# Kernel optimization log

Hardware: AMD Instinct MI355X
Metric: run time of the kernel (lower is better)

The kernel has to match this reference:

```python
import jax, jax.numpy as jnp
import numpy as np

EPS = 1e-6

def setup_inputs() -> dict:
    key = jax.random.key(0)
    k1, k2 = jax.random.split(key)
    S, B, H, F = 2048, 4, 2048, 8192
    x = jax.random.normal(k1, (S, B, H), dtype=jnp.float32)
    scale = jnp.ones((H,), dtype=jnp.float32)
    ln_bias = jnp.zeros((H,), dtype=jnp.float32)
    kernel = jax.random.normal(k2, (H, F), dtype=jnp.float32) * 0.02  # ~variance_scaling fan_in
    return {"x": x, "scale": scale, "ln_bias": ln_bias, "kernel": kernel}

def reference(x, scale, ln_bias, kernel):
    # LayerNorm over last (hidden) axis, stats in fp32
    mu = jnp.mean(x, axis=-1, keepdims=True)
    var = jnp.mean(jnp.square(x - mu), axis=-1, keepdims=True)
    y = (x - mu) * jax.lax.rsqrt(var + EPS) * scale + ln_bias  # [S,B,H]
    # Dense: contract hidden axis against kernel [H,F]
    z = jnp.einsum('sbh,hf->sbf', y, kernel)  # [S,B,F]
    # return_layernorm_output=True -> (dense_out, ln_out)
    return (z, y)
```

## Files before the change

kernel.cpp:

```cpp
#include <hip/hip_runtime.h>
#include <stdint.h>


typedef __attribute__((ext_vector_type(8))) short short8;
typedef __attribute__((ext_vector_type(4))) float floatx4;

__device__ __forceinline__ unsigned short f2bf(float f) {
    unsigned u = __builtin_bit_cast(unsigned, f);
    u += 0x7fffu + ((u >> 16) & 1u);
    return (unsigned short)(u >> 16);
}

__global__ __launch_bounds__(256) void ln_kernel(
    const float* __restrict__ x, const float* __restrict__ scale,
    const float* __restrict__ bias, float* __restrict__ y,
    unsigned short* __restrict__ ybf, int H)
{
    const int row = blockIdx.x;
    const float* xr = x + (size_t)row * H;
    const int tid = threadIdx.x;

    float4 v0 = ((const float4*)xr)[tid];
    float4 v1 = ((const float4*)xr)[tid + 256];

    float s  = v0.x + v0.y + v0.z + v0.w + v1.x + v1.y + v1.z + v1.w;
    float ss = v0.x*v0.x + v0.y*v0.y + v0.z*v0.z + v0.w*v0.w
             + v1.x*v1.x + v1.y*v1.y + v1.z*v1.z + v1.w*v1.w;

    #pragma unroll
    for (int off = 32; off > 0; off >>= 1) {
        s  += __shfl_down(s,  off, 64);
        ss += __shfl_down(ss, off, 64);
    }
    __shared__ float rs[4], rq[4];
    if ((tid & 63) == 0) { rs[tid >> 6] = s; rq[tid >> 6] = ss; }
    __syncthreads();
    float ts = rs[0] + rs[1] + rs[2] + rs[3];
    float tq = rq[0] + rq[1] + rq[2] + rq[3];
    float mean = ts / (float)H;
    float var  = tq / (float)H - mean * mean;
    float rstd = rsqrtf(var + 1e-6f);

    float4 sc0 = ((const float4*)scale)[tid];
    float4 sc1 = ((const float4*)scale)[tid + 256];
    float4 b0  = ((const float4*)bias)[tid];
    float4 b1  = ((const float4*)bias)[tid + 256];

    float4 o0, o1;
    o0.x = (v0.x - mean) * rstd * sc0.x + b0.x;
    o0.y = (v0.y - mean) * rstd * sc0.y + b0.y;
    o0.z = (v0.z - mean) * rstd * sc0.z + b0.z;
    o0.w = (v0.w - mean) * rstd * sc0.w + b0.w;
    o1.x = (v1.x - mean) * rstd * sc1.x + b1.x;
    o1.y = (v1.y - mean) * rstd * sc1.y + b1.y;
    o1.z = (v1.z - mean) * rstd * sc1.z + b1.z;
    o1.w = (v1.w - mean) * rstd * sc1.w + b1.w;

    float* yr = y + (size_t)row * H;
    ((float4*)yr)[tid]       = o0;
    ((float4*)yr)[tid + 256] = o1;

    unsigned short* br = ybf + (size_t)row * H;
    uint2 p0, p1;
    p0.x = (unsigned)f2bf(o0.x) | ((unsigned)f2bf(o0.y) << 16);
    p0.y = (unsigned)f2bf(o0.z) | ((unsigned)f2bf(o0.w) << 16);
    p1.x = (unsigned)f2bf(o1.x) | ((unsigned)f2bf(o1.y) << 16);
    p1.y = (unsigned)f2bf(o1.z) | ((unsigned)f2bf(o1.w) << 16);
    ((uint2*)br)[tid]       = p0;
    ((uint2*)br)[tid + 256] = p1;
}

__global__ __launch_bounds__(256) void transpose_cast_kernel(
    const float* __restrict__ W, unsigned short* __restrict__ Bt,
    int K, int F)
{
    __shared__ float tile[64][65];
    const int kBase = blockIdx.y * 64;
    const int fBase = blockIdx.x * 64;
    const int tid = threadIdx.x;

    #pragma unroll
    for (int p = 0; p < 4; ++p) {
        int kl = (tid >> 4) + p * 16;
        int fl = (tid & 15) * 4;
        float4 v = *(const float4*)&W[(size_t)(kBase + kl) * F + fBase + fl];
        tile[kl][fl]     = v.x;
        tile[kl][fl + 1] = v.y;
        tile[kl][fl + 2] = v.z;
        tile[kl][fl + 3] = v.w;
    }
    __syncthreads();

    #pragma unroll
    for (int p = 0; p < 2; ++p) {
        int fl = (tid >> 3) + p * 32;
        int k8 = (tid & 7) * 8;
        unsigned w[4];
        #pragma unroll
        for (int j = 0; j < 4; ++j) {
            unsigned lo = f2bf(tile[k8 + 2*j][fl]);
            unsigned hi = f2bf(tile[k8 + 2*j + 1][fl]);
            w[j] = lo | (hi << 16);
        }
        uint4 out = make_uint4(w[0], w[1], w[2], w[3]);
        *(uint4*)&Bt[(size_t)(fBase + fl) * K + kBase + k8] = out;
    }
}

#define GBM 256
#define GBN 256
#define GBK 32

__device__ __forceinline__ void gload16(const unsigned short* src,
                                        unsigned short* dst) {
    __builtin_amdgcn_global_load_lds(
        (const __attribute__((address_space(1))) unsigned int*)src,
        (__attribute__((address_space(3))) unsigned int*)dst, 16, 0, 0);
}

__device__ __forceinline__ void stage_op(
    const unsigned short* __restrict__ g, unsigned short* dst,
    int t, int K, int tid)
{
    #pragma unroll
    for (int i = 0; i < 2; ++i) {
        int e = i * 512 + tid;
        int r = e >> 2;
        int c = (e & 3) ^ ((r >> 1) & 3);
        gload16(g + (size_t)r * K + t * GBK + c * 8, dst + e * 8);
    }
}

__global__ __launch_bounds__(512, 2) void gemm_bf16_8w(
    const unsigned short* __restrict__ A,
    const unsigned short* __restrict__ Bt,
    float* __restrict__ C,
    int M, int N, int K)
{
    __shared__ __align__(128) unsigned short lds[4][16384];

    const int tid   = threadIdx.x;
    const int lane  = tid & 63;
    const int wave  = tid >> 6;
    const int waveM = wave >> 2;
    const int waveN = wave & 3;
    const int quad  = lane >> 4;
    const int l16   = lane & 15;
    const int soff  = (quad ^ ((l16 >> 1) & 3)) * 8;
    const int rowA0 = waveM * 128 + l16;
    const int rowB0 = waveN * 64 + l16;

    const int nwg = gridDim.x;
    const int cpx = nwg >> 3;
    const int bid = blockIdx.x;
    const int wg  = (bid & 7) * cpx + (bid >> 3);
    const int tilesN = N >> 8;
    const int tm = wg / tilesN;
    const int tn = wg % tilesN;

    const unsigned short* gA = A  + (size_t)tm * GBM * K;
    const unsigned short* gB = Bt + (size_t)tn * GBN * K;

    const int NT = K >> 5;

    floatx4 acc[8][4] = {};

    stage_op(gA, &lds[0][0],    0, K, tid);
    stage_op(gB, &lds[0][8192], 0, K, tid);
    stage_op(gA, &lds[1][0],    1, K, tid);
    stage_op(gB, &lds[1][8192], 1, K, tid);
    stage_op(gA, &lds[2][0],    2, K, tid);
    stage_op(gB, &lds[2][8192], 2, K, tid);
    asm volatile("s_waitcnt vmcnt(8)" ::: "memory");
    __builtin_amdgcn_s_barrier();

    for (int t = 0; t < NT; t += 4) {
        #pragma unroll
        for (int u = 0; u < 4; ++u) {
            const int tt = t + u;
            const unsigned short* bufA = &lds[u][0];
            const unsigned short* bufB = &lds[u][8192];
            unsigned short* pre = &lds[(u + 3) & 3][0];
            int ts = tt + 3; if (ts > NT - 1) ts = NT - 1;

            short8 a[4], b[4];
            #pragma unroll
            for (int i = 0; i < 4; ++i)
                a[i] = *(const short8*)(bufA + (rowA0 + i * 16) * 32 + soff);
            #pragma unroll
            for (int j = 0; j < 4; ++j)
                b[j] = *(const short8*)(bufB + (rowB0 + j * 16) * 32 + soff);
            stage_op(gA, pre, ts, K, tid);
            __builtin_amdgcn_sched_barrier(0);
            __builtin_amdgcn_s_barrier();
            asm volatile("s_waitcnt lgkmcnt(0)" ::: "memory");
            __builtin_amdgcn_sched_barrier(0);
            __builtin_amdgcn_s_setprio(1);
            #pragma unroll
            for (int i = 0; i < 4; ++i)
                #pragma unroll
                for (int j = 0; j < 4; ++j)
                    acc[i][j] = __builtin_amdgcn_mfma_f32_16x16x32_bf16(
                        a[i], b[j], acc[i][j], 0, 0, 0);
            __builtin_amdgcn_s_setprio(0);
            __builtin_amdgcn_s_barrier();

            #pragma unroll
            for (int i = 0; i < 4; ++i)
                a[i] = *(const short8*)(bufA + (rowA0 + 64 + i * 16) * 32 + soff);
            stage_op(gB, pre + 8192, ts, K, tid);
            __builtin_amdgcn_sched_barrier(0);
            __builtin_amdgcn_s_barrier();
            asm volatile("s_waitcnt lgkmcnt(0)" ::: "memory");
            __builtin_amdgcn_sched_barrier(0);
            __builtin_amdgcn_s_setprio(1);
            #pragma unroll
            for (int i = 0; i < 4; ++i)
                #pragma unroll
                for (int j = 0; j < 4; ++j)
                    acc[4 + i][j] = __builtin_amdgcn_mfma_f32_16x16x32_bf16(
                        a[i], b[j], acc[4 + i][j], 0, 0, 0);
            __builtin_amdgcn_s_setprio(0);
            asm volatile("s_waitcnt vmcnt(8)" ::: "memory");
            __builtin_amdgcn_s_barrier();
        }
    }

    const size_t bm = (size_t)tm * GBM;
    const size_t bn = (size_t)tn * GBN;
    #pragma unroll
    for (int mi = 0; mi < 8; ++mi) {
        #pragma unroll
        for (int ni = 0; ni < 4; ++ni) {
            size_t col = bn + (size_t)waveN * 64 + ni * 16 + l16;
            #pragma unroll
            for (int r = 0; r < 4; ++r) {
                size_t row = bm + (size_t)waveM * 128 + mi * 16 + quad * 4 + r;
                C[row * N + col] = acc[mi][ni][r];
            }
        }
    }
}

extern "C" void kernel_launch(void* const* d_in, const int* in_sizes, int n_in,
                              void* d_out, int out_size, void* d_ws, size_t ws_size,
                              hipStream_t stream) {
    const float* x      = (const float*)d_in[0];
    const float* scale  = (const float*)d_in[1];
    const float* lnbias = (const float*)d_in[2];
    const float* W      = (const float*)d_in[3];

    const int H = in_sizes[1];
    const int M = in_sizes[0] / H;
    const int F = in_sizes[3] / H;

    float* z = (float*)d_out;
    float* y = z + (size_t)M * F;

    unsigned short* Abf = (unsigned short*)d_ws;
    unsigned short* Btb = Abf + (size_t)M * H;

    ln_kernel<<<M, 256, 0, stream>>>(x, scale, lnbias, y, Abf, H);
    transpose_cast_kernel<<<dim3(F / 64, H / 64), 256, 0, stream>>>(W, Btb, H, F);
    gemm_bf16_8w<<<dim3((M / GBM) * (F / GBN)), 512, 0, stream>>>(Abf, Btb, z, M, F, H);
}
```

Baseline: 689.7 us.

## Software-pipeline GEMM LDS reads against MFMAs with register double buffering

Restructures the GEMM main loop so each stage reads the whole k-tile's A and B fragments from LDS into one register set while running MFMAs on the set loaded in the previous stage. The global-to-LDS prefetch distance drops from three tiles to two, and each stage now has one barrier instead of three. Offsets for the staging loads are precomputed once. The LayerNorm and transpose kernels switch to nontemporal loads and stores with vector arithmetic. The goal is to hide LDS latency behind MFMA work and cut synchronization, at the cost of roughly doubling fragment registers, which could cause spills at two blocks per CU.

```diff
diff --git a/kernel.cpp b/kernel.cpp
--- a/kernel.cpp
+++ b/kernel.cpp
@@ -4,6 +4,7 @@
 
 typedef __attribute__((ext_vector_type(8))) short short8;
 typedef __attribute__((ext_vector_type(4))) float floatx4;
+typedef __attribute__((ext_vector_type(4))) float f32x4;
 
 __device__ __forceinline__ unsigned short f2bf(float f) {
     unsigned u = __builtin_bit_cast(unsigned, f);
@@ -20,12 +21,12 @@
     const float* xr = x + (size_t)row * H;
     const int tid = threadIdx.x;
 
-    float4 v0 = ((const float4*)xr)[tid];
-    float4 v1 = ((const float4*)xr)[tid + 256];
-
-    float s  = v0.x + v0.y + v0.z + v0.w + v1.x + v1.y + v1.z + v1.w;
-    float ss = v0.x*v0.x + v0.y*v0.y + v0.z*v0.z + v0.w*v0.w
-             + v1.x*v1.x + v1.y*v1.y + v1.z*v1.z + v1.w*v1.w;
+    f32x4 v0 = __builtin_nontemporal_load((const f32x4*)xr + tid);
+    f32x4 v1 = __builtin_nontemporal_load((const f32x4*)xr + tid + 256);
+
+    float s  = v0[0] + v0[1] + v0[2] + v0[3] + v1[0] + v1[1] + v1[2] + v1[3];
+    float ss = v0[0]*v0[0] + v0[1]*v0[1] + v0[2]*v0[2] + v0[3]*v0[3]
+             + v1[0]*v1[0] + v1[1]*v1[1] + v1[2]*v1[2] + v1[3]*v1[3];
 
     #pragma unroll
     for (int off = 32; off > 0; off >>= 1) {
@@ -41,31 +42,24 @@
     float var  = tq / (float)H - mean * mean;
     float rstd = rsqrtf(var + 1e-6f);
 
-    float4 sc0 = ((const float4*)scale)[tid];
-    float4 sc1 = ((const float4*)scale)[tid + 256];
-    float4 b0  = ((const float4*)bias)[tid];
-    float4 b1  = ((const float4*)bias)[tid + 256];
-
-    float4 o0, o1;
-    o0.x = (v0.x - mean) * rstd * sc0.x + b0.x;
-    o0.y = (v0.y - mean) * rstd * sc0.y + b0.y;
-    o0.z = (v0.z - mean) * rstd * sc0.z + b0.z;
-    o0.w = (v0.w - mean) * rstd * sc0.w + b0.w;
-    o1.x = (v1.x - mean) * rstd * sc1.x + b1.x;
-    o1.y = (v1.y - mean) * rstd * sc1.y + b1.y;
-    o1.z = (v1.z - mean) * rstd * sc1.z + b1.z;
-    o1.w = (v1.w - mean) * rstd * sc1.w + b1.w;
+    f32x4 sc0 = ((const f32x4*)scale)[tid];
+    f32x4 sc1 = ((const f32x4*)scale)[tid + 256];
+    f32x4 b0  = ((const f32x4*)bias)[tid];
+    f32x4 b1  = ((const f32x4*)bias)[tid + 256];
+
+    f32x4 o0 = (v0 - mean) * rstd * sc0 + b0;
+    f32x4 o1 = (v1 - mean) * rstd * sc1 + b1;
 
     float* yr = y + (size_t)row * H;
-    ((float4*)yr)[tid]       = o0;
-    ((float4*)yr)[tid + 256] = o1;
+    __builtin_nontemporal_store(o0, (f32x4*)yr + tid);
+    __builtin_nontemporal_store(o1, (f32x4*)yr + tid + 256);
 
     unsigned short* br = ybf + (size_t)row * H;
     uint2 p0, p1;
-    p0.x = (unsigned)f2bf(o0.x) | ((unsigned)f2bf(o0.y) << 16);
-    p0.y = (unsigned)f2bf(o0.z) | ((unsigned)f2bf(o0.w) << 16);
-    p1.x = (unsigned)f2bf(o1.x) | ((unsigned)f2bf(o1.y) << 16);
-    p1.y = (unsigned)f2bf(o1.z) | ((unsigned)f2bf(o1.w) << 16);
+    p0.x = (unsigned)f2bf(o0[0]) | ((unsigned)f2bf(o0[1]) << 16);
+    p0.y = (unsigned)f2bf(o0[2]) | ((unsigned)f2bf(o0[3]) << 16);
+    p1.x = (unsigned)f2bf(o1[0]) | ((unsigned)f2bf(o1[1]) << 16);
+    p1.y = (unsigned)f2bf(o1[2]) | ((unsigned)f2bf(o1[3]) << 16);
     ((uint2*)br)[tid]       = p0;
     ((uint2*)br)[tid + 256] = p1;
 }
@@ -83,11 +77,12 @@
     for (int p = 0; p < 4; ++p) {
         int kl = (tid >> 4) + p * 16;
         int fl = (tid & 15) * 4;
-        float4 v = *(const float4*)&W[(size_t)(kBase + kl) * F + fBase + fl];
-        tile[kl][fl]     = v.x;
-        tile[kl][fl + 1] = v.y;
-        tile[kl][fl + 2] = v.z;
-        tile[kl][fl + 3] = v.w;
+        f32x4 v = __builtin_nontemporal_load(
+            (const f32x4*)&W[(size_t)(kBase + kl) * F + fBase + fl]);
+        tile[kl][fl]     = v[0];
+        tile[kl][fl + 1] = v[1];
+        tile[kl][fl + 2] = v[2];
+        tile[kl][fl + 3] = v[3];
     }
     __syncthreads();
 
@@ -116,19 +111,6 @@
     __builtin_amdgcn_global_load_lds(
         (const __attribute__((address_space(1))) unsigned int*)src,
         (__attribute__((address_space(3))) unsigned int*)dst, 16, 0, 0);
-}
-
-__device__ __forceinline__ void stage_op(
-    const unsigned short* __restrict__ g, unsigned short* dst,
-    int t, int K, int tid)
-{
-    #pragma unroll
-    for (int i = 0; i < 2; ++i) {
-        int e = i * 512 + tid;
-        int r = e >> 2;
-        int c = (e & 3) ^ ((r >> 1) & 3);
-        gload16(g + (size_t)r * K + t * GBK + c * 8, dst + e * 8);
-    }
 }
 
 __global__ __launch_bounds__(512, 2) void gemm_bf16_8w(
@@ -150,6 +132,16 @@
     const int rowA0 = waveM * 128 + l16;
     const int rowB0 = waveN * 64 + l16;
 
+    unsigned oo[2], dd[2];
+    #pragma unroll
+    for (int i = 0; i < 2; ++i) {
+        int e = i * 512 + tid;
+        int r = e >> 2;
+        int c = (e & 3) ^ ((r >> 1) & 3);
+        oo[i] = (unsigned)(r * K + c * 8);
+        dd[i] = (unsigned)(e * 8);
+    }
+
     const int nwg = gridDim.x;
     const int cpx = nwg >> 3;
     const int bid = blockIdx.x;
@@ -164,67 +156,101 @@
     const int NT = K >> 5;
 
     floatx4 acc[8][4] = {};
-
-    stage_op(gA, &lds[0][0],    0, K, tid);
-    stage_op(gB, &lds[0][8192], 0, K, tid);
-    stage_op(gA, &lds[1][0],    1, K, tid);
-    stage_op(gB, &lds[1][8192], 1, K, tid);
-    stage_op(gA, &lds[2][0],    2, K, tid);
-    stage_op(gB, &lds[2][8192], 2, K, tid);
-    asm volatile("s_waitcnt vmcnt(8)" ::: "memory");
+    short8 xa0[4], xa1[4], xb[4];
+    short8 ya0[4], ya1[4], yb[4];
+
+#define STAGE(ts, bu)                                                        \
+    do {                                                                     \
+        unsigned kb = (unsigned)(ts) * GBK;                                  \
+        gload16(gA + (oo[0] + kb), &lds[bu][0]    + dd[0]);                  \
+        gload16(gA + (oo[1] + kb), &lds[bu][0]    + dd[1]);                  \
+        gload16(gB + (oo[0] + kb), &lds[bu][8192] + dd[0]);                  \
+        gload16(gB + (oo[1] + kb), &lds[bu][8192] + dd[1]);                  \
+    } while (0)
+
+#define READF(bu, A0, A1, BB)                                                \
+    do {                                                                     \
+        const unsigned short* bA = &lds[bu][0]    + rowA0 * 32 + soff;       \
+        const unsigned short* bB = &lds[bu][8192] + rowB0 * 32 + soff;       \
+        _Pragma("unroll")                                                    \
+        for (int i = 0; i < 4; ++i) A0[i] = *(const short8*)(bA + i * 512);  \
+        _Pragma("unroll")                                                    \
+        for (int j = 0; j < 4; ++j) BB[j] = *(const short8*)(bB + j * 512);  \
+        _Pragma("unroll")                                                    \
+        for (int i = 0; i < 4; ++i) A1[i] = *(const short8*)(bA + 2048 + i * 512); \
+    } while (0)
+
+#define MFMAT(A0, A1, BB)                                                    \
+    do {                                                                     \
+        __builtin_amdgcn_s_setprio(1);                                       \
+        _Pragma("unroll")                                                    \
+        for (int i = 0; i < 4; ++i)                                          \
+            _Pragma("unroll")                                                \
+            for (int j = 0; j < 4; ++j)                                      \
+                acc[i][j] = __builtin_amdgcn_mfma_f32_16x16x32_bf16(         \
+                    A0[i], BB[j], acc[i][j], 0, 0, 0);                       \
+        _Pragma("unroll")                                                    \
+        for (int i = 0; i < 4; ++i)                                          \
+            _Pragma("unroll")                                                \
+            for (int j = 0; j < 4; ++j)                                      \
+                acc[4 + i][j] = __builtin_amdgcn_mfma_f32_16x16x32_bf16(     \
+                    A1[i], BB[j], acc[4 + i][j], 0, 0, 0);                   \
+        __builtin_amdgcn_s_setprio(0);                                       \
+    } while (0)
+
+    STAGE(0, 0);
+    STAGE(1, 1);
+    asm volatile("s_waitcnt vmcnt(4)" ::: "memory");
     __builtin_amdgcn_s_barrier();
 
     for (int t = 0; t < NT; t += 4) {
-        #pragma unroll
-        for (int u = 0; u < 4; ++u) {
-            const int tt = t + u;
-            const unsigned short* bufA = &lds[u][0];
-            const unsigned short* bufB = &lds[u][8192];
-            unsigned short* pre = &lds[(u + 3) & 3][0];
-            int ts = tt + 3; if (ts > NT - 1) ts = NT - 1;
-
-            short8 a[4], b[4];
-            #pragma unroll
-            for (int i = 0; i < 4; ++i)
-                a[i] = *(const short8*)(bufA + (rowA0 + i * 16) * 32 + soff);
-            #pragma unroll
-            for (int j = 0; j < 4; ++j)
-                b[j] = *(const short8*)(bufB + (rowB0 + j * 16) * 32 + soff);
-            stage_op(gA, pre, ts, K, tid);
-            __builtin_amdgcn_sched_barrier(0);
-            __builtin_amdgcn_s_barrier();
-            asm volatile("s_waitcnt lgkmcnt(0)" ::: "memory");
-            __builtin_amdgcn_sched_barrier(0);
-            __builtin_amdgcn_s_setprio(1);
-            #pragma unroll
-            for (int i = 0; i < 4; ++i)
-                #pragma unroll
-                for (int j = 0; j < 4; ++j)
-                    acc[i][j] = __builtin_amdgcn_mfma_f32_16x16x32_bf16(
-                        a[i], b[j], acc[i][j], 0, 0, 0);
-            __builtin_amdgcn_s_setprio(0);
-            __builtin_amdgcn_s_barrier();
-
-            #pragma unroll
-            for (int i = 0; i < 4; ++i)
-                a[i] = *(const short8*)(bufA + (rowA0 + 64 + i * 16) * 32 + soff);
-            stage_op(gB, pre + 8192, ts, K, tid);
-            __builtin_amdgcn_sched_barrier(0);
-            __builtin_amdgcn_s_barrier();
-            asm volatile("s_waitcnt lgkmcnt(0)" ::: "memory");
-            __builtin_amdgcn_sched_barrier(0);
-            __builtin_amdgcn_s_setprio(1);
-            #pragma unroll
-            for (int i = 0; i < 4; ++i)
-                #pragma unroll
-                for (int j = 0; j < 4; ++j)
-                    acc[4 + i][j] = __builtin_amdgcn_mfma_f32_16x16x32_bf16(
-                        a[i], b[j], acc[4 + i][j], 0, 0, 0);
-            __builtin_amdgcn_s_setprio(0);
-            asm volatile("s_waitcnt vmcnt(8)" ::: "memory");
-            __builtin_amdgcn_s_barrier();
-        }
-    }
+        {
+            int ts = t + 2; if (ts > NT - 1) ts = NT - 1;
+            STAGE(ts, 2);
+            READF(0, xa0, xa1, xb);
+            asm volatile("s_waitcnt lgkmcnt(12)" ::: "memory");
+            __builtin_amdgcn_sched_barrier(0);
+            if (t > 0) MFMAT(ya0, ya1, yb);
+            asm volatile("s_waitcnt vmcnt(4)" ::: "memory");
+            __builtin_amdgcn_s_barrier();
+        }
+        {
+            int ts = t + 3; if (ts > NT - 1) ts = NT - 1;
+            STAGE(ts, 3);
+            READF(1, ya0, ya1, yb);
+            asm volatile("s_waitcnt lgkmcnt(12)" ::: "memory");
+            __builtin_amdgcn_sched_barrier(0);
+            MFMAT(xa0, xa1, xb);
+            asm volatile("s_waitcnt vmcnt(4)" ::: "memory");
+            __builtin_amdgcn_s_barrier();
+        }
+        {
+            int ts = t + 4; if (ts > NT - 1) ts = NT - 1;
+            STAGE(ts, 0);
+            READF(2, xa0, xa1, xb);
+            asm volatile("s_waitcnt lgkmcnt(12)" ::: "memory");
+            __builtin_amdgcn_sched_barrier(0);
+            MFMAT(ya0, ya1, yb);
+            asm volatile("s_waitcnt vmcnt(4)" ::: "memory");
+            __builtin_amdgcn_s_barrier();
+        }
+        {
+            int ts = t + 5; if (ts > NT - 1) ts = NT - 1;
+            STAGE(ts, 1);
+            READF(3, ya0, ya1, yb);
+            asm volatile("s_waitcnt lgkmcnt(12)" ::: "memory");
+            __builtin_amdgcn_sched_barrier(0);
+            MFMAT(xa0, xa1, xb);
+            asm volatile("s_waitcnt vmcnt(4)" ::: "memory");
+            __builtin_amdgcn_s_barrier();
+        }
+    }
+    asm volatile("s_waitcnt lgkmcnt(0)" ::: "memory");
+    MFMAT(ya0, ya1, yb);
+
+#undef STAGE
+#undef READF
+#undef MFMAT
 
     const size_t bm = (size_t)tm * GBM;
     const size_t bn = (size_t)tn * GBN;
```

New measurement: 777.6 us. 12.7% more time.
